# Optimization experiments

Hardware: AMD Instinct MI355X
Metric: run time of the kernel (lower is better)

The kernel has to match this reference:

```python
import jax, jax.numpy as jnp
import numpy as np

B, N, K, C = 8, 4096, 16, 64
OUT = [128, 128, 128]
BN_EPS = 1e-3


def setup_inputs() -> dict:
    key = jax.random.key(0)
    ks = jax.random.split(key, 8)
    inp = {
        "points1": jax.random.normal(ks[0], (B, 3, N), jnp.float32),
        "points2": jax.random.normal(ks[1], (B, 3, N), jnp.float32),
        "features1": jax.random.normal(ks[2], (B, C, N), jnp.float32),
        "features2": jax.random.normal(ks[3], (B, C, N), jnp.float32),
    }
    dims = [2 * C + 3] + OUT  # [131, 128, 128, 128]
    for i in range(len(OUT)):
        kw = jax.random.fold_in(ks[4], i)
        inp[f"W{i}"] = jax.random.normal(kw, (dims[i + 1], dims[i]), jnp.float32) / np.sqrt(dims[i]).astype(np.float32)
        inp[f"b{i}"] = jnp.zeros((dims[i + 1],), jnp.float32)
        inp[f"gamma{i}"] = jnp.ones((dims[i + 1],), jnp.float32)
        inp[f"beta{i}"] = jnp.zeros((dims[i + 1],), jnp.float32)
    return inp


def _knn_group(points2, points1, features2):
    # points*: [B, 3, N].  For each query in points1, find K nearest in points2.
    d = jnp.sum((points1[:, :, :, None] - points2[:, :, None, :]) ** 2, axis=1)  # [B, Nq, Ns]
    _, idx = jax.lax.top_k(-d, K)  # [B, Nq, K]
    idx_b = idx[:, None, :, :]  # [B, 1, Nq, K] broadcasts over channel dim
    xyz_g = jnp.take_along_axis(points2[:, :, None, :], idx_b, axis=3)      # [B, 3, Nq, K]
    rel_xyz = xyz_g - points1[:, :, :, None]                                # relative coords
    feat_g = jnp.take_along_axis(features2[:, :, None, :], idx_b, axis=3)  # [B, C, Nq, K]
    return jnp.concatenate([rel_xyz, feat_g], axis=1)  # [B, C+3, Nq, K]


def _conv_bn_relu(x, W, b, gamma, beta):
    # 1x1 conv == per-position channel matmul; BN in training mode (batch stats, biased var)
    x = jnp.einsum('oc,bcnk->bonk', W, x) + b[None, :, None, None]
    mu = jnp.mean(x, axis=(0, 2, 3), keepdims=True)
    var = jnp.var(x, axis=(0, 2, 3), keepdims=True)
    x = (x - mu) * jax.lax.rsqrt(var + BN_EPS)
    x = x * gamma[None, :, None, None] + beta[None, :, None, None]
    return jax.nn.relu(x)


def reference(points1, points2, features1, features2,
              W0, b0, gamma0, beta0,
              W1, b1, gamma1, beta1,
              W2, b2, gamma2, beta2):
    g = _knn_group(points2, points1, features2)                       # [B, C+3, N, K]
    f1 = jnp.broadcast_to(features1[:, :, :, None], (B, C, N, K))     # expand over neighbors
    x = jnp.concatenate([g, f1], axis=1)                              # [B, 2C+3, N, K]
    x = _conv_bn_relu(x, W0, b0, gamma0, beta0)
    x = _conv_bn_relu(x, W1, b1, gamma1, beta1)
    x = _conv_bn_relu(x, W2, b2, gamma2, beta2)
    return jnp.max(x, axis=3)                                         # [B, OUT[-1], N]
```

## Files before the change

### kernel.cpp

```cpp
#include <hip/hip_runtime.h>

#define B_ 8
#define N_ 4096
#define K_ 16
#define C_ 64
#define NK_ (N_*K_)
#define M_ (B_*N_*K_)
#define BN_EPS_ 0.001f
#define CH_ 16
#define CS_ (N_/CH_)
#define Q_ (B_*N_)
#define NB1_ (M_/128)
#define NB0_ (M_/256)

typedef short bf16x8 __attribute__((ext_vector_type(8)));
typedef float f32x4 __attribute__((ext_vector_type(4)));

static __device__ __forceinline__ unsigned short f2bf(float x) {
  unsigned u = __float_as_uint(x);
  unsigned r = (u + 0x7FFFu + ((u >> 16) & 1u)) >> 16;
  return (unsigned short)r;
}
static __device__ __forceinline__ unsigned pk2bf(float a, float b) {
  return (unsigned)f2bf(a) | ((unsigned)f2bf(b) << 16);
}

__global__ __launch_bounds__(256) void pack_pts(const float* __restrict__ p,
                                                float4* __restrict__ pf4) {
  int i = blockIdx.x * 256 + threadIdx.x;
  int b = i >> 12;
  int n = i & (N_ - 1);
  const float* base = p + (size_t)b * 3 * N_;
  pf4[i] = make_float4(base[n], base[N_ + n], base[2 * N_ + n], 0.f);
}

__global__ __launch_bounds__(256) void wcvt(const float* __restrict__ W,
                                            unsigned short* __restrict__ Wb) {
  int i = blockIdx.x * 256 + threadIdx.x;
  Wb[i] = f2bf(W[i]);
}

__global__ void make_w0at(const float* __restrict__ W0, float* __restrict__ w0at) {
  int o = threadIdx.x;
  for (int d = 0; d < 3; ++d) w0at[d * 128 + o] = W0[o * 131 + d];
}

__global__ __launch_bounds__(64) void knn_part(const float4* __restrict__ p1f4,
                                               const float4* __restrict__ p2f4,
                                               float* __restrict__ pvals) {
  int lane = threadIdx.x;
  int blk = blockIdx.x;
  int chunk = blk & (CH_ - 1);
  int grp = (blk >> 4) & 63;
  int b = blk >> 10;
  int n1 = (grp << 6) + lane;
  int q = (b << 12) + n1;
  float4 qv = p1f4[q];
  float ax = qv.x, ay = qv.y, az = qv.z;
  const float4* pb = p2f4 + ((size_t)b << 12) + chunk * CS_;

  float s[16];
  #pragma unroll
  for (int i = 0; i < 16; ++i) s[i] = 3.0e38f;

  #pragma unroll 8
  for (int t = 0; t < CS_; ++t) {
    float4 c = pb[t];
    float dx = ax - c.x, dy = ay - c.y, dz = az - c.z;
    float d = __fadd_rn(__fadd_rn(__fmul_rn(dx, dx), __fmul_rn(dy, dy)), __fmul_rn(dz, dz));
    #pragma unroll
    for (int i = 0; i < 15; ++i) s[i] = __builtin_amdgcn_fmed3f(s[i], s[i + 1], d);
    s[15] = fminf(s[15], d);
  }
  #pragma unroll
  for (int i = 0; i < 16; ++i) pvals[(size_t)(chunk * 16 + i) * Q_ + q] = s[i];
}

__global__ __launch_bounds__(256) void knn_merge(const float* __restrict__ pvals,
                                                 float* __restrict__ Tarr) {
  int q = blockIdx.x * 256 + threadIdx.x;
  float s[16];
  #pragma unroll
  for (int i = 0; i < 16; ++i) s[i] = 3.0e38f;
  #pragma unroll 8
  for (int t = 0; t < CH_ * 16; ++t) {
    float d = pvals[(size_t)t * Q_ + q];
    #pragma unroll
    for (int i = 0; i < 15; ++i) s[i] = __builtin_amdgcn_fmed3f(s[i], s[i + 1], d);
    s[15] = fminf(s[15], d);
  }
  Tarr[q] = s[0];
}

__global__ __launch_bounds__(64) void knn_cand(const float4* __restrict__ p1f4,
                                               const float4* __restrict__ p2f4,
                                               const float* __restrict__ Tarr,
                                               int* __restrict__ cidx,
                                               int* __restrict__ ccnt) {
  int lane = threadIdx.x;
  int blk = blockIdx.x;
  int chunk = blk & (CH_ - 1);
  int grp = (blk >> 4) & 63;
  int b = blk >> 10;
  int n1 = (grp << 6) + lane;
  int q = (b << 12) + n1;
  float4 qq = p1f4[q];
  float ax = qq.x, ay = qq.y, az = qq.z;
  const float4* pb = p2f4 + ((size_t)b << 12) + chunk * CS_;
  float T = Tarr[q];
  int cnt = 0;
  int base = (q * CH_ + chunk) * 16;
  #pragma unroll 4
  for (int t = 0; t < CS_; ++t) {
    float4 c = pb[t];
    float dx = ax - c.x, dy = ay - c.y, dz = az - c.z;
    float d = __fadd_rn(__fadd_rn(__fmul_rn(dx, dx), __fmul_rn(dy, dy)), __fmul_rn(dz, dz));
    if (d <= T && cnt < 16) { cidx[base + cnt] = chunk * CS_ + t; ++cnt; }
  }
  ccnt[q * CH_ + chunk] = cnt;
}

__global__ __launch_bounds__(256) void knn_combine(const int* __restrict__ cidx,
                                                   const int* __restrict__ ccnt,
                                                   int* __restrict__ idxout) {
  int q = blockIdx.x * 256 + threadIdx.x;
  int tot = 0;
  int ob = q * 16;
  for (int c = 0; c < CH_; ++c) {
    int m = ccnt[q * CH_ + c];
    const int* src = cidx + (size_t)(q * CH_ + c) * 16;
    for (int i = 0; i < m && tot < 16; ++i) idxout[ob + tot++] = src[i];
  }
}

__global__ __launch_bounds__(256) void pkern(const float* __restrict__ f,
                                             const float* __restrict__ W0,
                                             const float* __restrict__ bias,
                                             float* __restrict__ P, int coff) {
  __shared__ float fx[32 * 65];
  __shared__ __align__(16) float Wl[64 * 132];
  int tid = threadIdx.x;
  int bn0 = blockIdx.x * 32;
  int b = bn0 >> 12, nb0 = bn0 & (N_ - 1);

  for (int u = tid; u < 32 * 64; u += 256) {
    int c = u >> 5, nl = u & 31;
    fx[nl * 65 + c] = f[((size_t)b * C_ + c) * N_ + nb0 + nl];
  }
  for (int u = tid; u < 128 * 64; u += 256) {
    int o = u >> 6, c = u & 63;
    Wl[c * 132 + o] = W0[o * 131 + coff + c];
  }
  __syncthreads();

  int og = tid & 15, np_ = tid >> 4;
  int o0 = og * 8;
  int na = np_ * 2, nb = na + 1;
  float acc0[8], acc1[8];
  #pragma unroll
  for (int j = 0; j < 8; ++j) {
    float bv = bias ? bias[o0 + j] : 0.f;
    acc0[j] = bv; acc1[j] = bv;
  }
  for (int c = 0; c < 64; ++c) {
    float x0 = fx[na * 65 + c], x1 = fx[nb * 65 + c];
    float4 wa = *(const float4*)&Wl[c * 132 + o0];
    float4 wb = *(const float4*)&Wl[c * 132 + o0 + 4];
    float w[8] = {wa.x, wa.y, wa.z, wa.w, wb.x, wb.y, wb.z, wb.w};
    #pragma unroll
    for (int j = 0; j < 8; ++j) {
      acc0[j] = fmaf(x0, w[j], acc0[j]);
      acc1[j] = fmaf(x1, w[j], acc1[j]);
    }
  }
  float* Pa = P + (size_t)(bn0 + na) * 128 + o0;
  float* Pb = P + (size_t)(bn0 + nb) * 128 + o0;
  *(float4*)Pa = make_float4(acc0[0], acc0[1], acc0[2], acc0[3]);
  *(float4*)(Pa + 4) = make_float4(acc0[4], acc0[5], acc0[6], acc0[7]);
  *(float4*)Pb = make_float4(acc1[0], acc1[1], acc1[2], acc1[3]);
  *(float4*)(Pb + 4) = make_float4(acc1[4], acc1[5], acc1[6], acc1[7]);
}

__global__ __launch_bounds__(256) void stats0_kernel(
    const float* __restrict__ P1, const float* __restrict__ P2,
    const int* __restrict__ idx, const float4* __restrict__ p1f4,
    const float4* __restrict__ p2f4, const float* __restrict__ w0at,
    float* __restrict__ part) {
  int tid = threadIdx.x;
  int c = tid & 127, h = tid >> 7;
  float w0 = w0at[c], w1 = w0at[128 + c], w2 = w0at[256 + c];
  float sum = 0.f, sq = 0.f;
  int rbase = blockIdx.x * 256 + h * 128;
  for (int i = 0; i < 128; ++i) {
    int r = rbase + i;
    int b = r >> 16;
    int nk = r & (NK_ - 1);
    int n = nk >> 4;
    int j = idx[r];
    float4 pq = p1f4[(b << 12) + n];
    float4 pj = p2f4[(b << 12) + j];
    float rx = pj.x - pq.x, ry = pj.y - pq.y, rz = pj.z - pq.z;
    float a0 = w0 * rx + w1 * ry + w2 * rz;
    float x = P1[(size_t)((b << 12) + n) * 128 + c] +
              P2[(size_t)((b << 12) + j) * 128 + c] + a0;
    sum += x;
    sq = fmaf(x, x, sq);
  }
  __shared__ float red[256 * 2];
  red[tid * 2] = sum;
  red[tid * 2 + 1] = sq;
  __syncthreads();
  if (h == 0) {
    float a = sum + red[(tid + 128) * 2];
    float q2 = sq + red[(tid + 128) * 2 + 1];
    part[(size_t)c * NB0_ + blockIdx.x] = a;
    part[(size_t)(128 + c) * NB0_ + blockIdx.x] = q2;
  }
}

__global__ __launch_bounds__(256) void reduce_stats(const float* __restrict__ part,
                                                    int nb, float* __restrict__ statso) {
  int s = blockIdx.x;
  int tid = threadIdx.x;
  const float* src = part + (size_t)s * nb;
  float a = 0.f;
  for (int i = tid; i < nb; i += 256) a += src[i];
  a += __shfl_xor(a, 1);  a += __shfl_xor(a, 2);  a += __shfl_xor(a, 4);
  a += __shfl_xor(a, 8);  a += __shfl_xor(a, 16); a += __shfl_xor(a, 32);
  __shared__ float red[4];
  if ((tid & 63) == 0) red[tid >> 6] = a;
  __syncthreads();
  if (tid == 0) statso[s] = red[0] + red[1] + red[2] + red[3];
}

__global__ void bnfin_kernel(const float* __restrict__ stats, const float* __restrict__ gamma,
                             const float* __restrict__ beta, float* __restrict__ bnp) {
  int o = threadIdx.x;
  const float invM = 1.0f / (float)M_;
  float mean = stats[o] * invM;
  float var = stats[128 + o] * invM - mean * mean;
  float s = gamma[o] * rsqrtf(var + BN_EPS_);
  bnp[o] = s;
  bnp[128 + o] = beta[o] - mean * s;
}

__global__ __launch_bounds__(256) void layer1_mfma(
    const float* __restrict__ P1, const float* __restrict__ P2,
    const int* __restrict__ idx, const float4* __restrict__ p1f4,
    const float4* __restrict__ p2f4, const float* __restrict__ w0at,
    const float* __restrict__ bnp0, const unsigned short* __restrict__ W1b,
    const float* __restrict__ b1, unsigned short* __restrict__ x1out,
    float* __restrict__ part) {
  __shared__ __align__(16) unsigned short Xs[128 * 136];
  __shared__ float sred[4 * 128 * 2];
  int tid = threadIdx.x;
  int R0 = blockIdx.x * 128;
  int b = R0 >> 16;
  int n0 = (R0 & (NK_ - 1)) >> 4;

  int cc = (tid & 15) * 8;
  int r0l = tid >> 4;

  {
    float wxv[8], wyv[8], wzv[8], svv[8], tvv[8];
    *(float4*)&wxv[0] = *(const float4*)(w0at + cc);       *(float4*)&wxv[4] = *(const float4*)(w0at + cc + 4);
    *(float4*)&wyv[0] = *(const float4*)(w0at + 128 + cc); *(float4*)&wyv[4] = *(const float4*)(w0at + 132 + cc);
    *(float4*)&wzv[0] = *(const float4*)(w0at + 256 + cc); *(float4*)&wzv[4] = *(const float4*)(w0at + 260 + cc);
    *(float4*)&svv[0] = *(const float4*)(bnp0 + cc);       *(float4*)&svv[4] = *(const float4*)(bnp0 + cc + 4);
    *(float4*)&tvv[0] = *(const float4*)(bnp0 + 128 + cc); *(float4*)&tvv[4] = *(const float4*)(bnp0 + 132 + cc);
    int jj[8];
    #pragma unroll
    for (int p = 0; p < 8; ++p) jj[p] = idx[R0 + r0l + p * 16];
    float4 pq8[8];
    #pragma unroll
    for (int p = 0; p < 8; ++p) pq8[p] = p1f4[(b << 12) + n0 + p];
    #pragma unroll
    for (int g = 0; g < 4; ++g) {
      float4 pjv[2], p1a[2], p1b[2], p2a[2], p2b[2];
      #pragma unroll
      for (int t = 0; t < 2; ++t) {
        int p = g * 2 + t;
        pjv[t] = p2f4[(b << 12) + jj[p]];
        const float* P1r = P1 + (size_t)((b << 12) + n0 + p) * 128 + cc;
        const float* P2r = P2 + (size_t)((b << 12) + jj[p]) * 128 + cc;
        p1a[t] = *(const float4*)P1r; p1b[t] = *(const float4*)(P1r + 4);
        p2a[t] = *(const float4*)P2r; p2b[t] = *(const float4*)(P2r + 4);
      }
      #pragma unroll
      for (int t = 0; t < 2; ++t) {
        int p = g * 2 + t;
        float rx = pjv[t].x - pq8[p].x, ry = pjv[t].y - pq8[p].y, rz = pjv[t].z - pq8[p].z;
        float p1v[8], p2v[8];
        *(float4*)&p1v[0] = p1a[t]; *(float4*)&p1v[4] = p1b[t];
        *(float4*)&p2v[0] = p2a[t]; *(float4*)&p2v[4] = p2b[t];
        float y[8];
        #pragma unroll
        for (int u = 0; u < 8; ++u) {
          float x = p1v[u] + p2v[u] + wxv[u] * rx + wyv[u] * ry + wzv[u] * rz;
          y[u] = fmaxf(fmaf(svv[u], x, tvv[u]), 0.f);
        }
        uint4 pk;
        pk.x = pk2bf(y[0], y[1]); pk.y = pk2bf(y[2], y[3]);
        pk.z = pk2bf(y[4], y[5]); pk.w = pk2bf(y[6], y[7]);
        *(uint4*)&Xs[(r0l + p * 16) * 136 + cc] = pk;
      }
    }
  }
  __syncthreads();

  int w = tid >> 6, lane = tid & 63;
  int m16 = lane & 15, qd = lane >> 4;
  f32x4 acc[2][8];
  #pragma unroll
  for (int mt = 0; mt < 2; ++mt)
    #pragma unroll
    for (int nt = 0; nt < 8; ++nt) acc[mt][nt] = (f32x4){0.f, 0.f, 0.f, 0.f};

  const unsigned short* Ab = &Xs[(w * 32 + m16) * 136 + qd * 8];
  const unsigned short* Bb = W1b + m16 * 128 + qd * 8;
  #pragma unroll 1
  for (int q = 0; q < 4; ++q) {
    bf16x8 A0 = *(const bf16x8*)(Ab + q * 32);
    bf16x8 A1 = *(const bf16x8*)(Ab + 16 * 136 + q * 32);
    #pragma unroll
    for (int nt = 0; nt < 8; ++nt) {
      bf16x8 Bv = *(const bf16x8*)(Bb + nt * 16 * 128 + q * 32);
      acc[0][nt] = __builtin_amdgcn_mfma_f32_16x16x32_bf16(A0, Bv, acc[0][nt], 0, 0, 0);
      acc[1][nt] = __builtin_amdgcn_mfma_f32_16x16x32_bf16(A1, Bv, acc[1][nt], 0, 0, 0);
    }
  }
  __syncthreads();

  float ssum[8], ssq[8];
  #pragma unroll
  for (int nt = 0; nt < 8; ++nt) { ssum[nt] = 0.f; ssq[nt] = 0.f; }
  #pragma unroll
  for (int nt = 0; nt < 8; ++nt) {
    int col = nt * 16 + m16;
    float bb = b1[col];
    #pragma unroll
    for (int mt = 0; mt < 2; ++mt) {
      #pragma unroll
      for (int rg = 0; rg < 4; ++rg) {
        float y = acc[mt][nt][rg] + bb;
        ssum[nt] += y;
        ssq[nt] = fmaf(y, y, ssq[nt]);
        Xs[(w * 32 + mt * 16 + qd * 4 + rg) * 136 + col] = f2bf(y);
      }
    }
  }
  #pragma unroll
  for (int nt = 0; nt < 8; ++nt) {
    ssum[nt] += __shfl_xor(ssum[nt], 16);
    ssum[nt] += __shfl_xor(ssum[nt], 32);
    ssq[nt] += __shfl_xor(ssq[nt], 16);
    ssq[nt] += __shfl_xor(ssq[nt], 32);
  }
  if (lane < 16) {
    #pragma unroll
    for (int nt = 0; nt < 8; ++nt) {
      sred[(w * 128 + nt * 16 + lane) * 2] = ssum[nt];
      sred[(w * 128 + nt * 16 + lane) * 2 + 1] = ssq[nt];
    }
  }
  __syncthreads();
  if (tid < 128) {
    float a = 0.f, q2 = 0.f;
    #pragma unroll
    for (int ww = 0; ww < 4; ++ww) {
      a += sred[(ww * 128 + tid) * 2];
      q2 += sred[(ww * 128 + tid) * 2 + 1];
    }
    part[(size_t)tid * NB1_ + blockIdx.x] = a;
    part[(size_t)(128 + tid) * NB1_ + blockIdx.x] = q2;
  }
  #pragma unroll
  for (int p = 0; p < 8; ++p) {
    int rl = r0l + p * 16;
    uint4 v = *(const uint4*)&Xs[rl * 136 + cc];
    *(uint4*)(x1out + (size_t)(R0 + rl) * 128 + cc) = v;
  }
}

__global__ __launch_bounds__(256) void layer2_mfma(
    const unsigned short* __restrict__ x1, const float* __restrict__ bnp1,
    const unsigned short* __restrict__ W2b, const float* __restrict__ b2,
    float* __restrict__ ymaxo, float* __restrict__ ymino,
    float* __restrict__ part) {
  __shared__ __align__(16) unsigned short Xs[128 * 136];
  __shared__ float sred[4 * 128 * 2];
  int tid = threadIdx.x;
  int R0 = blockIdx.x * 128;
  int b = R0 >> 16;
  int n0 = (R0 & (NK_ - 1)) >> 4;

  int cc = (tid & 15) * 8;
  int r0l = tid >> 4;

  {
    float svv[8], tvv[8];
    *(float4*)&svv[0] = *(const float4*)(bnp1 + cc);       *(float4*)&svv[4] = *(const float4*)(bnp1 + cc + 4);
    *(float4*)&tvv[0] = *(const float4*)(bnp1 + 128 + cc); *(float4*)&tvv[4] = *(const float4*)(bnp1 + 132 + cc);
    #pragma unroll
    for (int g = 0; g < 2; ++g) {
      uint4 pv[4];
      #pragma unroll
      for (int t = 0; t < 4; ++t)
        pv[t] = *(const uint4*)(x1 + (size_t)(R0 + r0l + (g * 4 + t) * 16) * 128 + cc);
      #pragma unroll
      for (int t = 0; t < 4; ++t) {
        int rl = r0l + (g * 4 + t) * 16;
        float xv[8];
        xv[0] = __uint_as_float(pv[t].x << 16); xv[1] = __uint_as_float(pv[t].x & 0xFFFF0000u);
        xv[2] = __uint_as_float(pv[t].y << 16); xv[3] = __uint_as_float(pv[t].y & 0xFFFF0000u);
        xv[4] = __uint_as_float(pv[t].z << 16); xv[5] = __uint_as_float(pv[t].z & 0xFFFF0000u);
        xv[6] = __uint_as_float(pv[t].w << 16); xv[7] = __uint_as_float(pv[t].w & 0xFFFF0000u);
        float y[8];
        #pragma unroll
        for (int u = 0; u < 8; ++u) y[u] = fmaxf(fmaf(svv[u], xv[u], tvv[u]), 0.f);
        uint4 pk;
        pk.x = pk2bf(y[0], y[1]); pk.y = pk2bf(y[2], y[3]);
        pk.z = pk2bf(y[4], y[5]); pk.w = pk2bf(y[6], y[7]);
        *(uint4*)&Xs[rl * 136 + cc] = pk;
      }
    }
  }
  __syncthreads();

  int w = tid >> 6, lane = tid & 63;
  int m16 = lane & 15, qd = lane >> 4;
  f32x4 acc[2][8];
  #pragma unroll
  for (int mt = 0; mt < 2; ++mt)
    #pragma unroll
    for (int nt = 0; nt < 8; ++nt) acc[mt][nt] = (f32x4){0.f, 0.f, 0.f, 0.f};

  const unsigned short* Ab = &Xs[(w * 32 + m16) * 136 + qd * 8];
  const unsigned short* Bb = W2b + m16 * 128 + qd * 8;
  #pragma unroll 1
  for (int q = 0; q < 4; ++q) {
    bf16x8 A0 = *(const bf16x8*)(Ab + q * 32);
    bf16x8 A1 = *(const bf16x8*)(Ab + 16 * 136 + q * 32);
    #pragma unroll
    for (int nt = 0; nt < 8; ++nt) {
      bf16x8 Bv = *(const bf16x8*)(Bb + nt * 16 * 128 + q * 32);
      acc[0][nt] = __builtin_amdgcn_mfma_f32_16x16x32_bf16(A0, Bv, acc[0][nt], 0, 0, 0);
      acc[1][nt] = __builtin_amdgcn_mfma_f32_16x16x32_bf16(A1, Bv, acc[1][nt], 0, 0, 0);
    }
  }

  float ssum[8], ssq[8], mxv[2][8], mnv[2][8];
  #pragma unroll
  for (int nt = 0; nt < 8; ++nt) { ssum[nt] = 0.f; ssq[nt] = 0.f; }
  #pragma unroll
  for (int nt = 0; nt < 8; ++nt) {
    float bb = b2[nt * 16 + m16];
    #pragma unroll
    for (int mt = 0; mt < 2; ++mt) {
      float y0 = acc[mt][nt][0] + bb;
      float mx = y0, mn = y0, su = y0, sq = y0 * y0;
      #pragma unroll
      for (int rg = 1; rg < 4; ++rg) {
        float y = acc[mt][nt][rg] + bb;
        mx = fmaxf(mx, y); mn = fminf(mn, y);
        su += y; sq = fmaf(y, y, sq);
      }
      mxv[mt][nt] = mx; mnv[mt][nt] = mn;
      ssum[nt] += su; ssq[nt] += sq;
    }
  }
  #pragma unroll
  for (int nt = 0; nt < 8; ++nt)
    #pragma unroll
    for (int mt = 0; mt < 2; ++mt) {
      mxv[mt][nt] = fmaxf(mxv[mt][nt], __shfl_xor(mxv[mt][nt], 16));
      mxv[mt][nt] = fmaxf(mxv[mt][nt], __shfl_xor(mxv[mt][nt], 32));
      mnv[mt][nt] = fminf(mnv[mt][nt], __shfl_xor(mnv[mt][nt], 16));
      mnv[mt][nt] = fminf(mnv[mt][nt], __shfl_xor(mnv[mt][nt], 32));
    }
  if (lane < 16) {
    #pragma unroll
    for (int mt = 0; mt < 2; ++mt) {
      int n = n0 + w * 2 + mt;
      size_t base = ((size_t)(b << 12) + n) * 128;
      #pragma unroll
      for (int nt = 0; nt < 8; ++nt) {
        ymaxo[base + nt * 16 + lane] = mxv[mt][nt];
        ymino[base + nt * 16 + lane] = mnv[mt][nt];
      }
    }
  }
  #pragma unroll
  for (int nt = 0; nt < 8; ++nt) {
    ssum[nt] += __shfl_xor(ssum[nt], 16);
    ssum[nt] += __shfl_xor(ssum[nt], 32);
    ssq[nt] += __shfl_xor(ssq[nt], 16);
    ssq[nt] += __shfl_xor(ssq[nt], 32);
  }
  if (lane < 16) {
    #pragma unroll
    for (int nt = 0; nt < 8; ++nt) {
      sred[(w * 128 + nt * 16 + lane) * 2] = ssum[nt];
      sred[(w * 128 + nt * 16 + lane) * 2 + 1] = ssq[nt];
    }
  }
  __syncthreads();
  if (tid < 128) {
    float a = 0.f, q2 = 0.f;
    #pragma unroll
    for (int ww = 0; ww < 4; ++ww) {
      a += sred[(ww * 128 + tid) * 2];
      q2 += sred[(ww * 128 + tid) * 2 + 1];
    }
    part[(size_t)tid * NB1_ + blockIdx.x] = a;
    part[(size_t)(128 + tid) * NB1_ + blockIdx.x] = q2;
  }
}

__global__ __launch_bounds__(256) void final_kernel(const float* __restrict__ ymaxo,
                                                    const float* __restrict__ ymino,
                                                    const float* __restrict__ bnp2,
                                                    float* __restrict__ out) {
  __shared__ float T[64 * 129];
  int tid = threadIdx.x;
  int b = blockIdx.x >> 6;
  int n0 = (blockIdx.x & 63) * 64;
  for (int u = tid; u < 64 * 128; u += 256) {
    int nl = u >> 7, o = u & 127;
    size_t base = ((size_t)(b << 12) + n0 + nl) * 128 + o;
    float s = bnp2[o], t = bnp2[128 + o];
    float v = fmaf(s, (s >= 0.f ? ymaxo[base] : ymino[base]), t);
    T[nl * 129 + o] = fmaxf(v, 0.f);
  }
  __syncthreads();
  for (int u = tid; u < 64 * 128; u += 256) {
    int o = u >> 6, nl = u & 63;
    out[((size_t)b * 128 + o) * N_ + n0 + nl] = T[nl * 129 + o];
  }
}

extern "C" void kernel_launch(void* const* d_in, const int* in_sizes, int n_in,
                              void* d_out, int out_size, void* d_ws, size_t ws_size,
                              hipStream_t stream) {
  (void)in_sizes; (void)n_in; (void)out_size; (void)ws_size;
  const float* points1 = (const float*)d_in[0];
  const float* points2 = (const float*)d_in[1];
  const float* features1 = (const float*)d_in[2];
  const float* features2 = (const float*)d_in[3];
  const float* W0 = (const float*)d_in[4];
  const float* b0 = (const float*)d_in[5];
  const float* g0 = (const float*)d_in[6];
  const float* be0 = (const float*)d_in[7];
  const float* W1 = (const float*)d_in[8];
  const float* b1 = (const float*)d_in[9];
  const float* g1 = (const float*)d_in[10];
  const float* be1 = (const float*)d_in[11];
  const float* W2 = (const float*)d_in[12];
  const float* b2 = (const float*)d_in[13];
  const float* g2 = (const float*)d_in[14];
  const float* be2 = (const float*)d_in[15];
  float* out = (float*)d_out;

  char* ws = (char*)d_ws;
  size_t off = 0;
  auto alloc = [&](size_t bytes) -> void* {
    void* p = ws + off;
    off += (bytes + 255) & ~(size_t)255;
    return p;
  };
  int* idx = (int*)alloc((size_t)M_ * 4);
  float4* p1f4 = (float4*)alloc((size_t)B_ * N_ * 16);
  float4* p2f4 = (float4*)alloc((size_t)B_ * N_ * 16);
  float* P1 = (float*)alloc((size_t)B_ * N_ * 128 * 4);
  float* P2 = (float*)alloc((size_t)B_ * N_ * 128 * 4);
  unsigned short* W1b = (unsigned short*)alloc(128 * 128 * 2);
  unsigned short* W2b = (unsigned short*)alloc(128 * 128 * 2);
  float* w0at = (float*)alloc(3 * 128 * 4);
  float* stats = (float*)alloc(3 * 256 * 4);
  float* bnp = (float*)alloc(3 * 256 * 4);
  unsigned short* x1 = (unsigned short*)alloc((size_t)M_ * 128 * 2);
  float* ymaxo = (float*)alloc((size_t)B_ * N_ * 128 * 4);
  float* ymino = (float*)alloc((size_t)B_ * N_ * 128 * 4);

  float* pvals = (float*)x1;
  int* cidx = (int*)((char*)x1 + (size_t)32 * 1024 * 1024);
  int* ccnt = (int*)((char*)x1 + (size_t)64 * 1024 * 1024);
  float* Tarr = (float*)((char*)x1 + (size_t)66 * 1024 * 1024);

  float* part0 = ymaxo;
  float* part1 = ymino;
  float* part2 = P1;

  pack_pts<<<B_ * N_ / 256, 256, 0, stream>>>(points1, p1f4);
  pack_pts<<<B_ * N_ / 256, 256, 0, stream>>>(points2, p2f4);
  wcvt<<<64, 256, 0, stream>>>(W1, W1b);
  wcvt<<<64, 256, 0, stream>>>(W2, W2b);
  make_w0at<<<1, 128, 0, stream>>>(W0, w0at);

  knn_part<<<B_ * 64 * CH_, 64, 0, stream>>>(p1f4, p2f4, pvals);
  knn_merge<<<Q_ / 256, 256, 0, stream>>>(pvals, Tarr);
  knn_cand<<<B_ * 64 * CH_, 64, 0, stream>>>(p1f4, p2f4, Tarr, cidx, ccnt);
  knn_combine<<<Q_ / 256, 256, 0, stream>>>(cidx, ccnt, idx);

  pkern<<<B_ * N_ / 32, 256, 0, stream>>>(features1, W0, b0, P1, 67);
  pkern<<<B_ * N_ / 32, 256, 0, stream>>>(features2, W0, nullptr, P2, 3);

  stats0_kernel<<<NB0_, 256, 0, stream>>>(P1, P2, idx, p1f4, p2f4, w0at, part0);
  reduce_stats<<<256, 256, 0, stream>>>(part0, NB0_, stats);
  bnfin_kernel<<<1, 128, 0, stream>>>(stats, g0, be0, bnp);

  layer1_mfma<<<NB1_, 256, 0, stream>>>(P1, P2, idx, p1f4, p2f4, w0at, bnp,
                                        W1b, b1, x1, part1);
  reduce_stats<<<256, 256, 0, stream>>>(part1, NB1_, stats + 256);
  bnfin_kernel<<<1, 128, 0, stream>>>(stats + 256, g1, be1, bnp + 256);

  layer2_mfma<<<NB1_, 256, 0, stream>>>(x1, bnp + 256, W2b, b2, ymaxo, ymino, part2);
  reduce_stats<<<256, 256, 0, stream>>>(part2, NB1_, stats + 512);
  bnfin_kernel<<<1, 128, 0, stream>>>(stats + 512, g2, be2, bnp + 512);

  final_kernel<<<B_ * N_ / 64, 256, 0, stream>>>(ymaxo, ymino, bnp + 512, out);
}
```

Baseline: 603.0 us.

## Recompute layer-1 activations inside layer-2 kernel instead of storing x1

The layer-1 kernel now only computes BN statistics and no longer writes the bf16 layer-1 activations to global memory. The layer-2 kernel re-gathers the layer-0 inputs, recomputes the layer-1 matmul, applies BN1 and ReLU in registers/LDS, then runs the layer-2 matmul. This removes a large intermediate write and read at the cost of a second gather pass and a duplicated MFMA GEMM. Scratch buffers that previously aliased x1 get their own allocations.

```diff
diff --git a/kernel.cpp b/kernel.cpp
--- a/kernel.cpp
+++ b/kernel.cpp
@@ -244,13 +244,12 @@
   bnp[128 + o] = beta[o] - mean * s;
 }
 
-__global__ __launch_bounds__(256) void layer1_mfma(
+__global__ __launch_bounds__(256) void layer1_stats(
     const float* __restrict__ P1, const float* __restrict__ P2,
     const int* __restrict__ idx, const float4* __restrict__ p1f4,
     const float4* __restrict__ p2f4, const float* __restrict__ w0at,
     const float* __restrict__ bnp0, const unsigned short* __restrict__ W1b,
-    const float* __restrict__ b1, unsigned short* __restrict__ x1out,
-    float* __restrict__ part) {
+    const float* __restrict__ b1, float* __restrict__ part) {
   __shared__ __align__(16) unsigned short Xs[128 * 136];
   __shared__ float sred[4 * 128 * 2];
   int tid = threadIdx.x;
@@ -329,15 +328,13 @@
       acc[1][nt] = __builtin_amdgcn_mfma_f32_16x16x32_bf16(A1, Bv, acc[1][nt], 0, 0, 0);
     }
   }
-  __syncthreads();
 
   float ssum[8], ssq[8];
   #pragma unroll
   for (int nt = 0; nt < 8; ++nt) { ssum[nt] = 0.f; ssq[nt] = 0.f; }
   #pragma unroll
   for (int nt = 0; nt < 8; ++nt) {
-    int col = nt * 16 + m16;
-    float bb = b1[col];
+    float bb = b1[nt * 16 + m16];
     #pragma unroll
     for (int mt = 0; mt < 2; ++mt) {
       #pragma unroll
@@ -345,7 +342,6 @@
         float y = acc[mt][nt][rg] + bb;
         ssum[nt] += y;
         ssq[nt] = fmaf(y, y, ssq[nt]);
-        Xs[(w * 32 + mt * 16 + qd * 4 + rg) * 136 + col] = f2bf(y);
       }
     }
   }
@@ -374,16 +370,14 @@
     part[(size_t)tid * NB1_ + blockIdx.x] = a;
     part[(size_t)(128 + tid) * NB1_ + blockIdx.x] = q2;
   }
-  #pragma unroll
-  for (int p = 0; p < 8; ++p) {
-    int rl = r0l + p * 16;
-    uint4 v = *(const uint4*)&Xs[rl * 136 + cc];
-    *(uint4*)(x1out + (size_t)(R0 + rl) * 128 + cc) = v;
-  }
-}
-
-__global__ __launch_bounds__(256) void layer2_mfma(
-    const unsigned short* __restrict__ x1, const float* __restrict__ bnp1,
+}
+
+__global__ __launch_bounds__(256) void layer2_fused(
+    const float* __restrict__ P1, const float* __restrict__ P2,
+    const int* __restrict__ idx, const float4* __restrict__ p1f4,
+    const float4* __restrict__ p2f4, const float* __restrict__ w0at,
+    const float* __restrict__ bnp0, const unsigned short* __restrict__ W1b,
+    const float* __restrict__ b1, const float* __restrict__ bnp1,
     const unsigned short* __restrict__ W2b, const float* __restrict__ b2,
     float* __restrict__ ymaxo, float* __restrict__ ymino,
     float* __restrict__ part) {
@@ -398,30 +392,47 @@
   int r0l = tid >> 4;
 
   {
-    float svv[8], tvv[8];
-    *(float4*)&svv[0] = *(const float4*)(bnp1 + cc);       *(float4*)&svv[4] = *(const float4*)(bnp1 + cc + 4);
-    *(float4*)&tvv[0] = *(const float4*)(bnp1 + 128 + cc); *(float4*)&tvv[4] = *(const float4*)(bnp1 + 132 + cc);
-    #pragma unroll
-    for (int g = 0; g < 2; ++g) {
-      uint4 pv[4];
-      #pragma unroll
-      for (int t = 0; t < 4; ++t)
-        pv[t] = *(const uint4*)(x1 + (size_t)(R0 + r0l + (g * 4 + t) * 16) * 128 + cc);
-      #pragma unroll
-      for (int t = 0; t < 4; ++t) {
-        int rl = r0l + (g * 4 + t) * 16;
-        float xv[8];
-        xv[0] = __uint_as_float(pv[t].x << 16); xv[1] = __uint_as_float(pv[t].x & 0xFFFF0000u);
-        xv[2] = __uint_as_float(pv[t].y << 16); xv[3] = __uint_as_float(pv[t].y & 0xFFFF0000u);
-        xv[4] = __uint_as_float(pv[t].z << 16); xv[5] = __uint_as_float(pv[t].z & 0xFFFF0000u);
-        xv[6] = __uint_as_float(pv[t].w << 16); xv[7] = __uint_as_float(pv[t].w & 0xFFFF0000u);
+    float wxv[8], wyv[8], wzv[8], svv[8], tvv[8];
+    *(float4*)&wxv[0] = *(const float4*)(w0at + cc);       *(float4*)&wxv[4] = *(const float4*)(w0at + cc + 4);
+    *(float4*)&wyv[0] = *(const float4*)(w0at + 128 + cc); *(float4*)&wyv[4] = *(const float4*)(w0at + 132 + cc);
+    *(float4*)&wzv[0] = *(const float4*)(w0at + 256 + cc); *(float4*)&wzv[4] = *(const float4*)(w0at + 260 + cc);
+    *(float4*)&svv[0] = *(const float4*)(bnp0 + cc);       *(float4*)&svv[4] = *(const float4*)(bnp0 + cc + 4);
+    *(float4*)&tvv[0] = *(const float4*)(bnp0 + 128 + cc); *(float4*)&tvv[4] = *(const float4*)(bnp0 + 132 + cc);
+    int jj[8];
+    #pragma unroll
+    for (int p = 0; p < 8; ++p) jj[p] = idx[R0 + r0l + p * 16];
+    float4 pq8[8];
+    #pragma unroll
+    for (int p = 0; p < 8; ++p) pq8[p] = p1f4[(b << 12) + n0 + p];
+    #pragma unroll
+    for (int g = 0; g < 4; ++g) {
+      float4 pjv[2], p1a[2], p1b[2], p2a[2], p2b[2];
+      #pragma unroll
+      for (int t = 0; t < 2; ++t) {
+        int p = g * 2 + t;
+        pjv[t] = p2f4[(b << 12) + jj[p]];
+        const float* P1r = P1 + (size_t)((b << 12) + n0 + p) * 128 + cc;
+        const float* P2r = P2 + (size_t)((b << 12) + jj[p]) * 128 + cc;
+        p1a[t] = *(const float4*)P1r; p1b[t] = *(const float4*)(P1r + 4);
+        p2a[t] = *(const float4*)P2r; p2b[t] = *(const float4*)(P2r + 4);
+      }
+      #pragma unroll
+      for (int t = 0; t < 2; ++t) {
+        int p = g * 2 + t;
+        float rx = pjv[t].x - pq8[p].x, ry = pjv[t].y - pq8[p].y, rz = pjv[t].z - pq8[p].z;
+        float p1v[8], p2v[8];
+        *(float4*)&p1v[0] = p1a[t]; *(float4*)&p1v[4] = p1b[t];
+        *(float4*)&p2v[0] = p2a[t]; *(float4*)&p2v[4] = p2b[t];
         float y[8];
         #pragma unroll
-        for (int u = 0; u < 8; ++u) y[u] = fmaxf(fmaf(svv[u], xv[u], tvv[u]), 0.f);
+        for (int u = 0; u < 8; ++u) {
+          float x = p1v[u] + p2v[u] + wxv[u] * rx + wyv[u] * ry + wzv[u] * rz;
+          y[u] = fmaxf(fmaf(svv[u], x, tvv[u]), 0.f);
+        }
         uint4 pk;
         pk.x = pk2bf(y[0], y[1]); pk.y = pk2bf(y[2], y[3]);
         pk.z = pk2bf(y[4], y[5]); pk.w = pk2bf(y[6], y[7]);
-        *(uint4*)&Xs[rl * 136 + cc] = pk;
+        *(uint4*)&Xs[(r0l + p * 16) * 136 + cc] = pk;
       }
     }
   }
@@ -436,7 +447,7 @@
     for (int nt = 0; nt < 8; ++nt) acc[mt][nt] = (f32x4){0.f, 0.f, 0.f, 0.f};
 
   const unsigned short* Ab = &Xs[(w * 32 + m16) * 136 + qd * 8];
-  const unsigned short* Bb = W2b + m16 * 128 + qd * 8;
+  const unsigned short* Bb = W1b + m16 * 128 + qd * 8;
   #pragma unroll 1
   for (int q = 0; q < 4; ++q) {
     bf16x8 A0 = *(const bf16x8*)(Ab + q * 32);
@@ -444,6 +455,41 @@
     #pragma unroll
     for (int nt = 0; nt < 8; ++nt) {
       bf16x8 Bv = *(const bf16x8*)(Bb + nt * 16 * 128 + q * 32);
+      acc[0][nt] = __builtin_amdgcn_mfma_f32_16x16x32_bf16(A0, Bv, acc[0][nt], 0, 0, 0);
+      acc[1][nt] = __builtin_amdgcn_mfma_f32_16x16x32_bf16(A1, Bv, acc[1][nt], 0, 0, 0);
+    }
+  }
+  __syncthreads();
+
+  #pragma unroll
+  for (int nt = 0; nt < 8; ++nt) {
+    int col = nt * 16 + m16;
+    float sc = bnp1[col];
+    float tc = fmaf(sc, b1[col], bnp1[128 + col]);
+    #pragma unroll
+    for (int mt = 0; mt < 2; ++mt) {
+      #pragma unroll
+      for (int rg = 0; rg < 4; ++rg) {
+        float y = fmaxf(fmaf(sc, acc[mt][nt][rg], tc), 0.f);
+        Xs[(w * 32 + mt * 16 + qd * 4 + rg) * 136 + col] = f2bf(y);
+      }
+    }
+  }
+  __syncthreads();
+
+  #pragma unroll
+  for (int mt = 0; mt < 2; ++mt)
+    #pragma unroll
+    for (int nt = 0; nt < 8; ++nt) acc[mt][nt] = (f32x4){0.f, 0.f, 0.f, 0.f};
+
+  const unsigned short* Bb2 = W2b + m16 * 128 + qd * 8;
+  #pragma unroll 1
+  for (int q = 0; q < 4; ++q) {
+    bf16x8 A0 = *(const bf16x8*)(Ab + q * 32);
+    bf16x8 A1 = *(const bf16x8*)(Ab + 16 * 136 + q * 32);
+    #pragma unroll
+    for (int nt = 0; nt < 8; ++nt) {
+      bf16x8 Bv = *(const bf16x8*)(Bb2 + nt * 16 * 128 + q * 32);
       acc[0][nt] = __builtin_amdgcn_mfma_f32_16x16x32_bf16(A0, Bv, acc[0][nt], 0, 0, 0);
       acc[1][nt] = __builtin_amdgcn_mfma_f32_16x16x32_bf16(A1, Bv, acc[1][nt], 0, 0, 0);
     }
@@ -578,18 +624,16 @@
   float* w0at = (float*)alloc(3 * 128 * 4);
   float* stats = (float*)alloc(3 * 256 * 4);
   float* bnp = (float*)alloc(3 * 256 * 4);
-  unsigned short* x1 = (unsigned short*)alloc((size_t)M_ * 128 * 2);
   float* ymaxo = (float*)alloc((size_t)B_ * N_ * 128 * 4);
   float* ymino = (float*)alloc((size_t)B_ * N_ * 128 * 4);
-
-  float* pvals = (float*)x1;
-  int* cidx = (int*)((char*)x1 + (size_t)32 * 1024 * 1024);
-  int* ccnt = (int*)((char*)x1 + (size_t)64 * 1024 * 1024);
-  float* Tarr = (float*)((char*)x1 + (size_t)66 * 1024 * 1024);
+  float* pvals = (float*)alloc((size_t)CH_ * 16 * Q_ * 4);
+  int* cidx = (int*)alloc((size_t)Q_ * CH_ * 16 * 4);
+  int* ccnt = (int*)alloc((size_t)Q_ * CH_ * 4);
+  float* Tarr = (float*)alloc((size_t)Q_ * 4);
 
   float* part0 = ymaxo;
   float* part1 = ymino;
-  float* part2 = P1;
+  float* part2 = pvals;
 
   pack_pts<<<B_ * N_ / 256, 256, 0, stream>>>(points1, p1f4);
   pack_pts<<<B_ * N_ / 256, 256, 0, stream>>>(points2, p2f4);
@@ -609,12 +653,14 @@
   reduce_stats<<<256, 256, 0, stream>>>(part0, NB0_, stats);
   bnfin_kernel<<<1, 128, 0, stream>>>(stats, g0, be0, bnp);
 
-  layer1_mfma<<<NB1_, 256, 0, stream>>>(P1, P2, idx, p1f4, p2f4, w0at, bnp,
-                                        W1b, b1, x1, part1);
+  layer1_stats<<<NB1_, 256, 0, stream>>>(P1, P2, idx, p1f4, p2f4, w0at, bnp,
+                                         W1b, b1, part1);
   reduce_stats<<<256, 256, 0, stream>>>(part1, NB1_, stats + 256);
   bnfin_kernel<<<1, 128, 0, stream>>>(stats + 256, g1, be1, bnp + 256);
 
-  layer2_mfma<<<NB1_, 256, 0, stream>>>(x1, bnp + 256, W2b, b2, ymaxo, ymino, part2);
+  layer2_fused<<<NB1_, 256, 0, stream>>>(P1, P2, idx, p1f4, p2f4, w0at, bnp,
+                                         W1b, b1, bnp + 256, W2b, b2,
+                                         ymaxo, ymino, part2);
   reduce_stats<<<256, 256, 0, stream>>>(part2, NB1_, stats + 512);
   bnfin_kernel<<<1, 128, 0, stream>>>(stats + 512, g2, be2, bnp + 512);
 
```

Result: slower. 676.2 us (+12.1%).
